# Performance work log

Hardware: AMD Instinct MI355X
Metric: run time of the kernel (lower is better)

Reference implementation:

```python
import jax, jax.numpy as jnp
import numpy as np

B, P, D = 64, 128, 1024  # batch, par_len, dim


def setup_inputs() -> dict:
    key = jax.random.key(0)
    k1, k2, k3, k4 = jax.random.split(key, 4)
    h = jax.random.normal(k1, (B, P, D), dtype=jnp.float32)
    q = jax.random.normal(k2, (B, P, D), dtype=jnp.float32)
    # Dense(1) over 2*dim features (attention score projection)
    W_att = jax.random.normal(k3, (2 * D, 1), dtype=jnp.float32) / np.sqrt(2 * D)
    b_att = jnp.zeros((1,), dtype=jnp.float32)
    # Determiner FC: Dense(2*dim -> output_size=1)
    W_fc = jax.random.normal(k4, (2 * D, 1), dtype=jnp.float32) / np.sqrt(2 * D)
    b_fc = jnp.zeros((1,), dtype=jnp.float32)
    return {"h": h, "q": q, "W_att": W_att, "b_att": b_att, "W_fc": W_fc, "b_fc": b_fc}


def reference(h, q, W_att, b_att, W_fc, b_fc):
    # Original builds x[b, i*P+j] = concat(h[b,i], q[b,i]) (independent of j),
    # scores it with Dense(1), softmaxes over P*P, and pools sum(a*x).
    # Since each score row is repeated P times, the P*P softmax + weighted sum
    # is exactly softmax over P of the per-i score, applied to c[b,i].
    c = jnp.concatenate([h, q], axis=-1)                 # (B, P, 2D)
    s = jnp.einsum('bpd,d->bp', c, W_att[:, 0]) + b_att  # (B, P)
    p = jax.nn.softmax(s, axis=1)                        # (B, P)
    y = jnp.einsum('bp,bpd->bd', p, c)                   # (B, 2D)
    return y @ W_fc + b_fc                               # (B, 1)
```

## Files before the change

kernel.cpp:

```cpp
#include <hip/hip_runtime.h>
#include <hip/hip_bf16.h>


#define BB 64
#define PP 128
#define DD 1024

__global__ __launch_bounds__(256) void score_kernel(
    const float* __restrict__ h,
    const float* __restrict__ q,
    const float* __restrict__ Watt,
    const float* __restrict__ Wfc,
    float* __restrict__ s_out, float* __restrict__ t_out)
{
    const int r   = blockIdx.x;
    const int tid = threadIdx.x;
    const bool isq = tid >= 128;
    const int j = tid & 127;

    const float* row = (isq ? q : h) + (size_t)r * DD;
    const float* wa  = Watt + (isq ? DD : 0);
    const float* wf  = Wfc  + (isq ? DD : 0);

    const float4* row4 = (const float4*)row;
    const float4* wa4  = (const float4*)wa;
    const float4* wf4  = (const float4*)wf;

    float s_acc = 0.f, t_acc = 0.f;
    #pragma unroll
    for (int c = 0; c < 2; ++c) {
        const int idx = j + c * 128;
        float4 x = row4[idx];
        float4 a = wa4[idx];
        float4 f = wf4[idx];
        s_acc += x.x*a.x + x.y*a.y + x.z*a.z + x.w*a.w;
        t_acc += x.x*f.x + x.y*f.y + x.z*f.z + x.w*f.w;
    }

    #pragma unroll
    for (int off = 32; off > 0; off >>= 1) {
        s_acc += __shfl_down(s_acc, off, 64);
        t_acc += __shfl_down(t_acc, off, 64);
    }

    __shared__ float sh_s[4], sh_t[4];
    const int wave = tid >> 6;
    if ((tid & 63) == 0) { sh_s[wave] = s_acc; sh_t[wave] = t_acc; }
    __syncthreads();
    if (tid == 0) {
        s_out[r] = sh_s[0] + sh_s[1] + sh_s[2] + sh_s[3];
        t_out[r] = sh_t[0] + sh_t[1] + sh_t[2] + sh_t[3];
    }
}

__global__ __launch_bounds__(128) void softmax_pool_kernel(
    const float* __restrict__ s_in, const float* __restrict__ t_in,
    const float* __restrict__ b_fc,
    float* __restrict__ out)
{
    const int b = blockIdx.x;
    const int p = threadIdx.x;
    const float s = s_in[b * PP + p];
    const float t = t_in[b * PP + p];

    float m = s;
    #pragma unroll
    for (int off = 32; off > 0; off >>= 1) m = fmaxf(m, __shfl_down(m, off, 64));
    __shared__ float sh_m[2];
    if ((p & 63) == 0) sh_m[p >> 6] = m;
    __syncthreads();
    m = fmaxf(sh_m[0], sh_m[1]);

    float e   = __expf(s - m);
    float num = e * t;
    #pragma unroll
    for (int off = 32; off > 0; off >>= 1) {
        e   += __shfl_down(e, off, 64);
        num += __shfl_down(num, off, 64);
    }
    __shared__ float sh_z[2], sh_n[2];
    if ((p & 63) == 0) { sh_z[p >> 6] = e; sh_n[p >> 6] = num; }
    __syncthreads();
    if (p == 0) {
        const float Z = sh_z[0] + sh_z[1];
        const float N = sh_n[0] + sh_n[1];
        out[b] = N / Z + b_fc[0];
    }
}

extern "C" void kernel_launch(void* const* d_in, const int* in_sizes, int n_in,
                              void* d_out, int out_size, void* d_ws, size_t ws_size,
                              hipStream_t stream) {
    const float* h     = (const float*)d_in[0];
    const float* q     = (const float*)d_in[1];
    const float* W_att = (const float*)d_in[2];
    const float* W_fc  = (const float*)d_in[4];
    const float* b_fc  = (const float*)d_in[5];

    float* s_ws = (float*)d_ws;
    float* t_ws = s_ws + BB * PP;

    score_kernel<<<BB * PP, 256, 0, stream>>>(h, q, W_att, W_fc, s_ws, t_ws);
    softmax_pool_kernel<<<BB, 128, 0, stream>>>(s_ws, t_ws, b_fc, (float*)d_out);
}
```

Measured before the change: 99.73 us.

## Fuse score and softmax-pool into one cooperative kernel with grid sync

Merges the two launches into a single cooperative kernel: 1024 blocks each score 8 rows, reusing the weight vectors held in registers, then all blocks meet at a grid-wide barrier and the first 64 blocks do the softmax pooling. This removes one kernel launch and cuts redundant weight loads per row. In exchange it adds a grid sync and needs all 1024 blocks to be co-resident, which the cooperative launch requires and which may fail or serialize if occupancy is too low.

Measured after the change: 176.2 us. 76.7% more time.

```diff
diff --git a/kernel.cpp b/kernel.cpp
--- a/kernel.cpp
+++ b/kernel.cpp
@@ -1,75 +1,81 @@
 #include <hip/hip_runtime.h>
-#include <hip/hip_bf16.h>
+#include <hip/hip_cooperative_groups.h>
+
+namespace cg = cooperative_groups;
 
 
 #define BB 64
 #define PP 128
 #define DD 1024
+#define NBLK 1024
+#define RPB 8
 
-__global__ __launch_bounds__(256) void score_kernel(
+__global__ __launch_bounds__(256, 4) void fused_kernel(
     const float* __restrict__ h,
     const float* __restrict__ q,
     const float* __restrict__ Watt,
     const float* __restrict__ Wfc,
-    float* __restrict__ s_out, float* __restrict__ t_out)
+    const float* __restrict__ b_fc,
+    float* __restrict__ s_ws,
+    float* __restrict__ t_ws,
+    float* __restrict__ out)
 {
-    const int r   = blockIdx.x;
-    const int tid = threadIdx.x;
-    const bool isq = tid >= 128;
-    const int j = tid & 127;
+    const int  tid  = threadIdx.x;
+    const bool isq  = tid >= 128;
+    const int  j    = tid & 127;
+    const int  wave = tid >> 6;
+    const int  lane = tid & 63;
 
-    const float* row = (isq ? q : h) + (size_t)r * DD;
-    const float* wa  = Watt + (isq ? DD : 0);
-    const float* wf  = Wfc  + (isq ? DD : 0);
+    {
+        const float4* wa4 = (const float4*)(Watt + (isq ? DD : 0));
+        const float4* wf4 = (const float4*)(Wfc  + (isq ? DD : 0));
+        const float4 wa0 = wa4[j], wa1 = wa4[j + 128];
+        const float4 wf0 = wf4[j], wf1 = wf4[j + 128];
 
-    const float4* row4 = (const float4*)row;
-    const float4* wa4  = (const float4*)wa;
-    const float4* wf4  = (const float4*)wf;
+        const float* base = isq ? q : h;
+        const int r0 = blockIdx.x * RPB;
 
-    float s_acc = 0.f, t_acc = 0.f;
-    #pragma unroll
-    for (int c = 0; c < 2; ++c) {
-        const int idx = j + c * 128;
-        float4 x = row4[idx];
-        float4 a = wa4[idx];
-        float4 f = wf4[idx];
-        s_acc += x.x*a.x + x.y*a.y + x.z*a.z + x.w*a.w;
-        t_acc += x.x*f.x + x.y*f.y + x.z*f.z + x.w*f.w;
+        __shared__ float sh_s[RPB][4], sh_t[RPB][4];
+
+        #pragma unroll
+        for (int k = 0; k < RPB; ++k) {
+            const float4* row4 = (const float4*)(base + (size_t)(r0 + k) * DD);
+            const float4 x0 = row4[j];
+            const float4 x1 = row4[j + 128];
+            float s = x0.x*wa0.x + x0.y*wa0.y + x0.z*wa0.z + x0.w*wa0.w
+                    + x1.x*wa1.x + x1.y*wa1.y + x1.z*wa1.z + x1.w*wa1.w;
+            float t = x0.x*wf0.x + x0.y*wf0.y + x0.z*wf0.z + x0.w*wf0.w
+                    + x1.x*wf1.x + x1.y*wf1.y + x1.z*wf1.z + x1.w*wf1.w;
+            #pragma unroll
+            for (int off = 32; off > 0; off >>= 1) {
+                s += __shfl_down(s, off, 64);
+                t += __shfl_down(t, off, 64);
+            }
+            if (lane == 0) { sh_s[k][wave] = s; sh_t[k][wave] = t; }
+        }
+        __syncthreads();
+        if (tid < RPB) {
+            const int r = blockIdx.x * RPB + tid;
+            s_ws[r] = sh_s[tid][0] + sh_s[tid][1] + sh_s[tid][2] + sh_s[tid][3];
+            t_ws[r] = sh_t[tid][0] + sh_t[tid][1] + sh_t[tid][2] + sh_t[tid][3];
+        }
     }
 
-    #pragma unroll
-    for (int off = 32; off > 0; off >>= 1) {
-        s_acc += __shfl_down(s_acc, off, 64);
-        t_acc += __shfl_down(t_acc, off, 64);
-    }
+    cg::this_grid().sync();
 
-    __shared__ float sh_s[4], sh_t[4];
-    const int wave = tid >> 6;
-    if ((tid & 63) == 0) { sh_s[wave] = s_acc; sh_t[wave] = t_acc; }
-    __syncthreads();
-    if (tid == 0) {
-        s_out[r] = sh_s[0] + sh_s[1] + sh_s[2] + sh_s[3];
-        t_out[r] = sh_t[0] + sh_t[1] + sh_t[2] + sh_t[3];
-    }
-}
+    if (blockIdx.x >= BB) return;
+    const int b = blockIdx.x;
 
-__global__ __launch_bounds__(128) void softmax_pool_kernel(
-    const float* __restrict__ s_in, const float* __restrict__ t_in,
-    const float* __restrict__ b_fc,
-    float* __restrict__ out)
-{
-    const int b = blockIdx.x;
-    const int p = threadIdx.x;
-    const float s = s_in[b * PP + p];
-    const float t = t_in[b * PP + p];
+    float s = -INFINITY, t = 0.f;
+    if (tid < PP) { s = s_ws[b * PP + tid]; t = t_ws[b * PP + tid]; }
 
     float m = s;
     #pragma unroll
     for (int off = 32; off > 0; off >>= 1) m = fmaxf(m, __shfl_down(m, off, 64));
-    __shared__ float sh_m[2];
-    if ((p & 63) == 0) sh_m[p >> 6] = m;
+    __shared__ float sh_m[4], sh_z[4], sh_n[4];
+    if (lane == 0) sh_m[wave] = m;
     __syncthreads();
-    m = fmaxf(sh_m[0], sh_m[1]);
+    m = fmaxf(fmaxf(sh_m[0], sh_m[1]), fmaxf(sh_m[2], sh_m[3]));
 
     float e   = __expf(s - m);
     float num = e * t;
@@ -78,12 +84,11 @@
         e   += __shfl_down(e, off, 64);
         num += __shfl_down(num, off, 64);
     }
-    __shared__ float sh_z[2], sh_n[2];
-    if ((p & 63) == 0) { sh_z[p >> 6] = e; sh_n[p >> 6] = num; }
+    if (lane == 0) { sh_z[wave] = e; sh_n[wave] = num; }
     __syncthreads();
-    if (p == 0) {
-        const float Z = sh_z[0] + sh_z[1];
-        const float N = sh_n[0] + sh_n[1];
+    if (tid == 0) {
+        const float Z = sh_z[0] + sh_z[1] + sh_z[2] + sh_z[3];
+        const float N = sh_n[0] + sh_n[1] + sh_n[2] + sh_n[3];
         out[b] = N / Z + b_fc[0];
     }
 }
@@ -99,7 +104,10 @@
 
     float* s_ws = (float*)d_ws;
     float* t_ws = s_ws + BB * PP;
+    float* outp = (float*)d_out;
 
-    score_kernel<<<BB * PP, 256, 0, stream>>>(h, q, W_att, W_fc, s_ws, t_ws);
-    softmax_pool_kernel<<<BB, 128, 0, stream>>>(s_ws, t_ws, b_fc, (float*)d_out);
+    void* args[] = {(void*)&h, (void*)&q, (void*)&W_att, (void*)&W_fc,
+                    (void*)&b_fc, (void*)&s_ws, (void*)&t_ws, (void*)&outp};
+    hipLaunchCooperativeKernel((const void*)fused_kernel,
+                               dim3(NBLK), dim3(256), args, 0, stream);
 }
```
